# Optimization experiments

Measured on AMD Instinct MI355X. Metric: run time of the kernel, lower is better.

## Reference

```python
import jax, jax.numpy as jnp
import numpy as np

TEMP = 50.0  # softmax temperature from __init__ (temp=50.0)

N_SAMPLES = 32768
NUM_CANDIDATES = 2048
NUM_DIMS = 16


def setup_inputs() -> dict:
    key = jax.random.key(0)
    k1, k2, k3 = jax.random.split(key, 3)
    X = jax.random.normal(k1, (N_SAMPLES, NUM_DIMS), dtype=jnp.float32)
    Y = jax.random.normal(k2, (1, NUM_CANDIDATES, NUM_DIMS), dtype=jnp.float32)  # Y_rest param
    b = jax.random.normal(k3, (1, NUM_CANDIDATES), dtype=jnp.float32) * 0.1     # intercept_rest param
    return {"X": X, "Y": Y, "b": b}


def reference(X, Y, b):
    """FiniteModel.forward in convex mode with soft selection.

    scores[n, c] = <X[n], Y[0, c]> - b[0, c]           (dot-product kernel)
    weights      = softmax(temp * scores, axis=1)       (moded_max, soft mode)
    f_x[n]       = sum_c weights[n, c] * scores[n, c]
    choice[n, :] = sum_c weights[n, c] * Y[0, c, :]
    Returns (choice, f_x) as in the torch forward.
    """
    Yc = Y[0]                                     # [C, D]
    scores = jnp.einsum('nd,cd->nc', X, Yc) - b   # [N, C] (b broadcasts from [1, C])
    weights = jax.nn.softmax(TEMP * scores, axis=1)
    f_x = jnp.sum(weights * scores, axis=1)       # [N]
    choice = jnp.einsum('nc,cd->nd', weights, Yc) # [N, D]
    return choice, f_x
```

## Files before the change

kernel.cpp:

```cpp
#include <hip/hip_runtime.h>
#include <math.h>

#if defined(__has_builtin)
#  if __has_builtin(__builtin_amdgcn_exp2f)
#    define EXP2F(x) __builtin_amdgcn_exp2f(x)
#  else
#    define EXP2F(x) exp2f(x)
#  endif
#else
#  define EXP2F(x) exp2f(x)
#endif

constexpr int   DD = 16;
constexpr float T2 = 72.13475204444817f;
constexpr float DEFER_THR = 8.0f;

typedef __attribute__((ext_vector_type(8)))  short s16x8;
typedef __attribute__((ext_vector_type(16))) float f32x16;

static __device__ __forceinline__ s16x8 mk8(unsigned a, unsigned b, unsigned c, unsigned d) {
    union { unsigned u[4]; s16x8 v; } x;
    x.u[0] = a; x.u[1] = b; x.u[2] = c; x.u[3] = d;
    return x.v;
}
static __device__ __forceinline__ unsigned pack_tr(float a, float b) {
    return (__float_as_uint(a) >> 16) | (__float_as_uint(b) & 0xFFFF0000u);
}
static __device__ __forceinline__ float trunc_bf(float a) {
    return __uint_as_float(__float_as_uint(a) & 0xFFFF0000u);
}
static __device__ __forceinline__ unsigned short rne16(float f) {
    unsigned u = __float_as_uint(f);
    return (unsigned short)((u + 0x7FFFu + ((u >> 16) & 1u)) >> 16);
}
static __device__ __forceinline__ float bfh2f(unsigned short h) {
    return __uint_as_float(((unsigned)h) << 16);
}

__global__ void prep_kernel(const float* __restrict__ Y, const float* __restrict__ B,
                            unsigned short* __restrict__ YhA, unsigned short* __restrict__ YlA,
                            unsigned short* __restrict__ VhP, unsigned short* __restrict__ VlP,
                            unsigned* __restrict__ Bq, int C)
{
    int c = blockIdx.x * blockDim.x + threadIdx.x;
    if (c >= C) return;

    int c15 = c & 15;
    int j    = (c15 & 3) | (((c15 >> 3) & 1) << 2);
    int hslt = (c15 >> 2) & 1;
    int slot = (c & ~15) | (hslt << 3) | j;

    const float* yr = Y + (size_t)c * DD;
#pragma unroll
    for (int d = 0; d < DD; ++d) {
        float y = yr[d];
        unsigned short h = rne16(y);
        unsigned short l = rne16(y - bfh2f(h));
        YhA[(size_t)c * DD + d] = h;
        YlA[(size_t)c * DD + d] = l;
        VhP[(size_t)d * C + slot] = h;
        VlP[(size_t)d * C + slot] = l;
    }
    float bb = B[c];
    unsigned short bh = rne16(bb);
    VhP[(size_t)16 * C + slot] = bh;
    VlP[(size_t)16 * C + slot] = rne16(bb - bfh2f(bh));
    VhP[(size_t)17 * C + slot] = 0x3F80;
    VlP[(size_t)17 * C + slot] = 0;
#pragma unroll
    for (int r = 18; r < 32; ++r) {
        VhP[(size_t)r * C + slot] = 0;
        VlP[(size_t)r * C + slot] = 0;
    }

    float qb = -T2 * bb;
    unsigned short qh = rne16(qb);
    unsigned short ql = rne16(qb - bfh2f(qh));
    Bq[c] = (unsigned)qh | ((unsigned)ql << 16);
}

struct Frag {
    s16x8 aYh, aYl, vh0, vh1, vl0, vl1;
    unsigned bw;
};

__global__ __launch_bounds__(256, 4)
void finite_mfma(const float* __restrict__ X,
                 const unsigned short* __restrict__ YhA, const unsigned short* __restrict__ YlA,
                 const unsigned short* __restrict__ VhP, const unsigned short* __restrict__ VlP,
                 const unsigned* __restrict__ Bq,
                 float* __restrict__ out, int N, int C)
{
    const int tid  = threadIdx.x;
    const int wave = tid >> 6, lane = tid & 63;
    const int s = lane & 31, hi = lane >> 5;
    const int n0 = blockIdx.x * 32;
    const int cpw = C >> 2, cbase = wave * cpw, ntile = cpw >> 5;

    __shared__ float bufc[4][18][32];
    __shared__ float lds_m[4][32];

    const unsigned short* pYh = YhA + ((size_t)(cbase + s) * DD + 8 * hi);
    const unsigned short* pYl = YlA + ((size_t)(cbase + s) * DD + 8 * hi);
    const unsigned short* pVh = VhP + ((size_t)s * C + cbase + 8 * hi);
    const unsigned short* pVl = VlP + ((size_t)s * C + cbase + 8 * hi);
    const unsigned*       pBq = Bq + cbase + s;

    const float* xp = X + ((size_t)(n0 + s) * DD + 8 * hi);
    float xq[8];
#pragma unroll
    for (int jj = 0; jj < 8; ++jj) xq[jj] = xp[jj] * T2;
    unsigned xhw[4], xlw[4];
#pragma unroll
    for (int jj = 0; jj < 4; ++jj) {
        float a = xq[2 * jj], b = xq[2 * jj + 1];
        xhw[jj] = pack_tr(a, b);
        xlw[jj] = pack_tr(a - trunc_bf(a), b - trunc_bf(b));
    }
    const s16x8 xqh = mk8(xhw[0], xhw[1], xhw[2], xhw[3]);
    const s16x8 xql = mk8(xlw[0], xlw[1], xlw[2], xlw[3]);
    const s16x8 ones2 = mk8(hi ? 0u : 0x3F803F80u, 0u, 0u, 0u);

    f32x16 acc;
#pragma unroll
    for (int r = 0; r < 16; ++r) acc[r] = 0.0f;
    float m2 = -INFINITY;

#define LDF(F, k) do {                                              \
        (F).aYh = *(const s16x8*)(pYh + (size_t)(k) * 512);         \
        (F).aYl = *(const s16x8*)(pYl + (size_t)(k) * 512);         \
        (F).vh0 = *(const s16x8*)(pVh + (size_t)(k) * 32);          \
        (F).vh1 = *(const s16x8*)(pVh + (size_t)(k) * 32 + 16);     \
        (F).vl0 = *(const s16x8*)(pVl + (size_t)(k) * 32);          \
        (F).vl1 = *(const s16x8*)(pVl + (size_t)(k) * 32 + 16);     \
        (F).bw  = pBq[(size_t)(k) * 32];                            \
    } while (0)

#define PROC(F) do {                                                            \
        const s16x8 a2 = mk8(hi ? 0u : (F).bw, 0u, 0u, 0u);                     \
        f32x16 S;                                                               \
        _Pragma("unroll")                                                       \
        for (int r = 0; r < 16; ++r) S[r] = 0.0f;                               \
        S = __builtin_amdgcn_mfma_f32_32x32x16_bf16(a2,     ones2, S, 0, 0, 0); \
        S = __builtin_amdgcn_mfma_f32_32x32x16_bf16((F).aYh, xqh,  S, 0, 0, 0); \
        S = __builtin_amdgcn_mfma_f32_32x32x16_bf16((F).aYh, xql,  S, 0, 0, 0); \
        S = __builtin_amdgcn_mfma_f32_32x32x16_bf16((F).aYl, xqh,  S, 0, 0, 0); \
        float tmax = S[0];                                                      \
        _Pragma("unroll")                                                       \
        for (int r = 1; r < 16; ++r) tmax = fmaxf(tmax, S[r]);                  \
        tmax = fmaxf(tmax, __shfl_xor(tmax, 32, 64));                           \
        if (__any(tmax > m2 + DEFER_THR)) {                                     \
            float nm = fmaxf(m2, tmax);                                         \
            float sc = EXP2F(m2 - nm);                                          \
            _Pragma("unroll")                                                   \
            for (int r = 0; r < 16; ++r) acc[r] *= sc;                          \
            m2 = nm;                                                            \
        }                                                                       \
        unsigned phw[8], plw[8];                                                \
        _Pragma("unroll")                                                       \
        for (int jj = 0; jj < 8; ++jj) {                                        \
            float e0 = EXP2F(S[2 * jj] - m2);                                   \
            float e1 = EXP2F(S[2 * jj + 1] - m2);                               \
            phw[jj] = pack_tr(e0, e1);                                          \
            plw[jj] = pack_tr(e0 - trunc_bf(e0), e1 - trunc_bf(e1));            \
        }                                                                       \
        const s16x8 Bph0 = mk8(phw[0], phw[1], phw[2], phw[3]);                 \
        const s16x8 Bpl0 = mk8(plw[0], plw[1], plw[2], plw[3]);                 \
        const s16x8 Bph1 = mk8(phw[4], phw[5], phw[6], phw[7]);                 \
        const s16x8 Bpl1 = mk8(plw[4], plw[5], plw[6], plw[7]);                 \
        acc = __builtin_amdgcn_mfma_f32_32x32x16_bf16((F).vh0, Bph0, acc, 0, 0, 0); \
        acc = __builtin_amdgcn_mfma_f32_32x32x16_bf16((F).vl0, Bph0, acc, 0, 0, 0); \
        acc = __builtin_amdgcn_mfma_f32_32x32x16_bf16((F).vh0, Bpl0, acc, 0, 0, 0); \
        acc = __builtin_amdgcn_mfma_f32_32x32x16_bf16((F).vh1, Bph1, acc, 0, 0, 0); \
        acc = __builtin_amdgcn_mfma_f32_32x32x16_bf16((F).vl1, Bph1, acc, 0, 0, 0); \
        acc = __builtin_amdgcn_mfma_f32_32x32x16_bf16((F).vh1, Bpl1, acc, 0, 0, 0); \
    } while (0)

    Frag f0, f1;
    LDF(f0, 0);
    for (int t = 0; t < ntile; t += 2) {
        LDF(f1, t + 1);
        PROC(f0);
        if (t + 2 < ntile) LDF(f0, t + 2);
        PROC(f1);
    }
#undef LDF
#undef PROC

    if (hi == 0) lds_m[wave][s] = m2;
    __syncthreads();
    float mstar = fmaxf(fmaxf(lds_m[0][s], lds_m[1][s]), fmaxf(lds_m[2][s], lds_m[3][s]));
    float sw = EXP2F(m2 - mstar);
#pragma unroll
    for (int r = 0; r < 8; ++r) {
        int dv = (r & 3) + 8 * (r >> 2) + 4 * hi;
        bufc[wave][dv][s] = acc[r] * sw;
    }
    if (hi == 0) {
        bufc[wave][16][s] = acc[8] * sw;
        bufc[wave][17][s] = acc[9] * sw;
    }
    __syncthreads();

#pragma unroll
    for (int q = 0; q < 3; ++q) {
        int u = tid + 256 * q;
        if (u < 18 * 32) {
            int dv = u >> 5, ss = u & 31;
            bufc[0][dv][ss] = bufc[0][dv][ss] + bufc[1][dv][ss]
                            + bufc[2][dv][ss] + bufc[3][dv][ss];
        }
    }
    __syncthreads();

    {
        int ss = tid >> 3, d0 = (tid & 7) * 2;
        float inv = 1.0f / bufc[0][17][ss];
        float2 o = make_float2(bufc[0][d0][ss] * inv, bufc[0][d0 + 1][ss] * inv);
        *(float2*)(out + (size_t)(n0 + ss) * DD + d0) = o;
    }
    if (tid < 32) {
        float inv = 1.0f / bufc[0][17][tid];
        const float* xr = X + (size_t)(n0 + tid) * DD;
        float dot = 0.0f;
#pragma unroll
        for (int d = 0; d < DD; ++d) dot = fmaf(xr[d], bufc[0][d][tid], dot);
        out[(size_t)N * DD + n0 + tid] = (dot - bufc[0][16][tid]) * inv;
    }
}

extern "C" void kernel_launch(void* const* d_in, const int* in_sizes, int n_in,
                              void* d_out, int out_size, void* d_ws, size_t ws_size,
                              hipStream_t stream) {
    const float* X = (const float*)d_in[0];
    const float* Y = (const float*)d_in[1];
    const float* B = (const float*)d_in[2];
    float*     out = (float*)d_out;

    const int N = in_sizes[0] / DD;
    const int C = in_sizes[2];

    char* w = (char*)d_ws;
    unsigned short* YhA = (unsigned short*)(w);
    unsigned short* YlA = (unsigned short*)(w + (size_t)C * DD * 2);
    unsigned short* VhP = (unsigned short*)(w + (size_t)C * DD * 4);
    unsigned short* VlP = (unsigned short*)(w + (size_t)C * DD * 4 + (size_t)32 * C * 2);
    unsigned*       Bq  = (unsigned*)   (w + (size_t)C * DD * 4 + (size_t)32 * C * 4);

    hipLaunchKernelGGL(prep_kernel, dim3((C + 255) / 256), dim3(256), 0, stream,
                       Y, B, YhA, YlA, VhP, VlP, Bq, C);
    hipLaunchKernelGGL(finite_mfma, dim3(N / 32), dim3(256), 0, stream,
                       X, YhA, YlA, VhP, VlP, Bq, out, N, C);
}
```

Measured before the change: 95.73 us.

## Drop low-part softmax weight MFMAs and retile V into per-tile contiguous layout

Removes the bf16 low-part split of the exponentiated weights, cutting the second-stage MFMAs per tile from six to four and dropping the residual packing ALU work. The V operand is re-laid out so each 32-candidate tile is a contiguous 32x32 block, written with vector stores in prep and read with contiguous loads in the main kernel. The per-tile max reduction becomes a tree instead of a linear chain. Accuracy of the weighted sums drops, since the weights now carry only bf16 precision.

Result: faster. 86.74 us (-9.4%).

```diff
diff --git a/kernel.cpp b/kernel.cpp
--- a/kernel.cpp
+++ b/kernel.cpp
@@ -39,44 +39,51 @@
 
 __global__ void prep_kernel(const float* __restrict__ Y, const float* __restrict__ B,
                             unsigned short* __restrict__ YhA, unsigned short* __restrict__ YlA,
-                            unsigned short* __restrict__ VhP, unsigned short* __restrict__ VlP,
+                            unsigned short* __restrict__ V3h, unsigned short* __restrict__ V3l,
                             unsigned* __restrict__ Bq, int C)
 {
     int c = blockIdx.x * blockDim.x + threadIdx.x;
     if (c >= C) return;
 
-    int c15 = c & 15;
-    int j    = (c15 & 3) | (((c15 >> 3) & 1) << 2);
-    int hslt = (c15 >> 2) & 1;
-    int slot = (c & ~15) | (hslt << 3) | j;
-
+    union { unsigned short u[DD]; s16x8 v[2]; } hb, lb;
     const float* yr = Y + (size_t)c * DD;
 #pragma unroll
     for (int d = 0; d < DD; ++d) {
         float y = yr[d];
         unsigned short h = rne16(y);
-        unsigned short l = rne16(y - bfh2f(h));
-        YhA[(size_t)c * DD + d] = h;
-        YlA[(size_t)c * DD + d] = l;
-        VhP[(size_t)d * C + slot] = h;
-        VlP[(size_t)d * C + slot] = l;
-    }
+        hb.u[d] = h;
+        lb.u[d] = rne16(y - bfh2f(h));
+    }
+    s16x8* yh = (s16x8*)(YhA + (size_t)c * DD);
+    s16x8* yl = (s16x8*)(YlA + (size_t)c * DD);
+    yh[0] = hb.v[0]; yh[1] = hb.v[1];
+    yl[0] = lb.v[0]; yl[1] = lb.v[1];
+
     float bb = B[c];
-    unsigned short bh = rne16(bb);
-    VhP[(size_t)16 * C + slot] = bh;
-    VlP[(size_t)16 * C + slot] = rne16(bb - bfh2f(bh));
-    VhP[(size_t)17 * C + slot] = 0x3F80;
-    VlP[(size_t)17 * C + slot] = 0;
-#pragma unroll
-    for (int r = 18; r < 32; ++r) {
-        VhP[(size_t)r * C + slot] = 0;
-        VlP[(size_t)r * C + slot] = 0;
-    }
-
     float qb = -T2 * bb;
     unsigned short qh = rne16(qb);
-    unsigned short ql = rne16(qb - bfh2f(qh));
-    Bq[c] = (unsigned)qh | ((unsigned)ql << 16);
+    Bq[c] = (unsigned)qh | ((unsigned)rne16(qb - bfh2f(qh)) << 16);
+
+    const int t = c >> 5, r = c & 31;
+    union { unsigned short u[32]; s16x8 v[4]; } vh, vl;
+#pragma unroll
+    for (int slot = 0; slot < 32; ++slot) {
+        int j = slot & 7, hs = (slot >> 3) & 1;
+        int cl = (slot & 16) | (j & 3) | (hs << 2) | (((j >> 2) & 1) << 3);
+        int cc = (t << 5) | cl;
+        float v;
+        if (r < DD)            v = Y[(size_t)cc * DD + r];
+        else if (r == DD)      v = B[cc];
+        else if (r == DD + 1)  v = 1.0f;
+        else                   v = 0.0f;
+        unsigned short h = rne16(v);
+        vh.u[slot] = h;
+        vl.u[slot] = rne16(v - bfh2f(h));
+    }
+    s16x8* ph = (s16x8*)(V3h + ((size_t)t * 32 + r) * 32);
+    s16x8* pl = (s16x8*)(V3l + ((size_t)t * 32 + r) * 32);
+#pragma unroll
+    for (int q = 0; q < 4; ++q) { ph[q] = vh.v[q]; pl[q] = vl.v[q]; }
 }
 
 struct Frag {
@@ -87,7 +94,7 @@
 __global__ __launch_bounds__(256, 4)
 void finite_mfma(const float* __restrict__ X,
                  const unsigned short* __restrict__ YhA, const unsigned short* __restrict__ YlA,
-                 const unsigned short* __restrict__ VhP, const unsigned short* __restrict__ VlP,
+                 const unsigned short* __restrict__ V3h, const unsigned short* __restrict__ V3l,
                  const unsigned* __restrict__ Bq,
                  float* __restrict__ out, int N, int C)
 {
@@ -102,8 +109,8 @@
 
     const unsigned short* pYh = YhA + ((size_t)(cbase + s) * DD + 8 * hi);
     const unsigned short* pYl = YlA + ((size_t)(cbase + s) * DD + 8 * hi);
-    const unsigned short* pVh = VhP + ((size_t)s * C + cbase + 8 * hi);
-    const unsigned short* pVl = VlP + ((size_t)s * C + cbase + 8 * hi);
+    const unsigned short* pVh = V3h + (((size_t)(cbase >> 5) * 32 + s) * 32 + 8 * hi);
+    const unsigned short* pVl = V3l + (((size_t)(cbase >> 5) * 32 + s) * 32 + 8 * hi);
     const unsigned*       pBq = Bq + cbase + s;
 
     const float* xp = X + ((size_t)(n0 + s) * DD + 8 * hi);
@@ -129,10 +136,10 @@
 #define LDF(F, k) do {                                              \
         (F).aYh = *(const s16x8*)(pYh + (size_t)(k) * 512);         \
         (F).aYl = *(const s16x8*)(pYl + (size_t)(k) * 512);         \
-        (F).vh0 = *(const s16x8*)(pVh + (size_t)(k) * 32);          \
-        (F).vh1 = *(const s16x8*)(pVh + (size_t)(k) * 32 + 16);     \
-        (F).vl0 = *(const s16x8*)(pVl + (size_t)(k) * 32);          \
-        (F).vl1 = *(const s16x8*)(pVl + (size_t)(k) * 32 + 16);     \
+        (F).vh0 = *(const s16x8*)(pVh + (size_t)(k) * 1024);        \
+        (F).vh1 = *(const s16x8*)(pVh + (size_t)(k) * 1024 + 16);   \
+        (F).vl0 = *(const s16x8*)(pVl + (size_t)(k) * 1024);        \
+        (F).vl1 = *(const s16x8*)(pVl + (size_t)(k) * 1024 + 16);   \
         (F).bw  = pBq[(size_t)(k) * 32];                            \
     } while (0)
 
@@ -145,10 +152,13 @@
         S = __builtin_amdgcn_mfma_f32_32x32x16_bf16((F).aYh, xqh,  S, 0, 0, 0); \
         S = __builtin_amdgcn_mfma_f32_32x32x16_bf16((F).aYh, xql,  S, 0, 0, 0); \
         S = __builtin_amdgcn_mfma_f32_32x32x16_bf16((F).aYl, xqh,  S, 0, 0, 0); \
-        float tmax = S[0];                                                      \
-        _Pragma("unroll")                                                       \
-        for (int r = 1; r < 16; ++r) tmax = fmaxf(tmax, S[r]);                  \
-        tmax = fmaxf(tmax, __shfl_xor(tmax, 32, 64));                           \
+        float tm[8];                                                            \
+        _Pragma("unroll")                                                       \
+        for (int jj = 0; jj < 8; ++jj) tm[jj] = fmaxf(S[2 * jj], S[2 * jj + 1]);\
+        _Pragma("unroll")                                                       \
+        for (int jj = 0; jj < 4; ++jj) tm[jj] = fmaxf(tm[jj], tm[jj + 4]);      \
+        tm[0] = fmaxf(fmaxf(tm[0], tm[2]), fmaxf(tm[1], tm[3]));                \
+        float tmax = fmaxf(tm[0], __shfl_xor(tm[0], 32, 64));                   \
         if (__any(tmax > m2 + DEFER_THR)) {                                     \
             float nm = fmaxf(m2, tmax);                                         \
             float sc = EXP2F(m2 - nm);                                          \
@@ -156,24 +166,19 @@
             for (int r = 0; r < 16; ++r) acc[r] *= sc;                          \
             m2 = nm;                                                            \
         }                                                                       \
-        unsigned phw[8], plw[8];                                                \
+        unsigned phw[8];                                                        \
         _Pragma("unroll")                                                       \
         for (int jj = 0; jj < 8; ++jj) {                                        \
             float e0 = EXP2F(S[2 * jj] - m2);                                   \
             float e1 = EXP2F(S[2 * jj + 1] - m2);                               \
             phw[jj] = pack_tr(e0, e1);                                          \
-            plw[jj] = pack_tr(e0 - trunc_bf(e0), e1 - trunc_bf(e1));            \
         }                                                                       \
         const s16x8 Bph0 = mk8(phw[0], phw[1], phw[2], phw[3]);                 \
-        const s16x8 Bpl0 = mk8(plw[0], plw[1], plw[2], plw[3]);                 \
         const s16x8 Bph1 = mk8(phw[4], phw[5], phw[6], phw[7]);                 \
-        const s16x8 Bpl1 = mk8(plw[4], plw[5], plw[6], plw[7]);                 \
         acc = __builtin_amdgcn_mfma_f32_32x32x16_bf16((F).vh0, Bph0, acc, 0, 0, 0); \
         acc = __builtin_amdgcn_mfma_f32_32x32x16_bf16((F).vl0, Bph0, acc, 0, 0, 0); \
-        acc = __builtin_amdgcn_mfma_f32_32x32x16_bf16((F).vh0, Bpl0, acc, 0, 0, 0); \
         acc = __builtin_amdgcn_mfma_f32_32x32x16_bf16((F).vh1, Bph1, acc, 0, 0, 0); \
         acc = __builtin_amdgcn_mfma_f32_32x32x16_bf16((F).vl1, Bph1, acc, 0, 0, 0); \
-        acc = __builtin_amdgcn_mfma_f32_32x32x16_bf16((F).vh1, Bpl1, acc, 0, 0, 0); \
     } while (0)
 
     Frag f0, f1;
@@ -243,12 +248,12 @@
     char* w = (char*)d_ws;
     unsigned short* YhA = (unsigned short*)(w);
     unsigned short* YlA = (unsigned short*)(w + (size_t)C * DD * 2);
-    unsigned short* VhP = (unsigned short*)(w + (size_t)C * DD * 4);
-    unsigned short* VlP = (unsigned short*)(w + (size_t)C * DD * 4 + (size_t)32 * C * 2);
+    unsigned short* V3h = (unsigned short*)(w + (size_t)C * DD * 4);
+    unsigned short* V3l = (unsigned short*)(w + (size_t)C * DD * 4 + (size_t)32 * C * 2);
     unsigned*       Bq  = (unsigned*)   (w + (size_t)C * DD * 4 + (size_t)32 * C * 4);
 
     hipLaunchKernelGGL(prep_kernel, dim3((C + 255) / 256), dim3(256), 0, stream,
-                       Y, B, YhA, YlA, VhP, VlP, Bq, C);
+                       Y, B, YhA, YlA, V3h, V3l, Bq, C);
     hipLaunchKernelGGL(finite_mfma, dim3(N / 32), dim3(256), 0, stream,
-                       X, YhA, YlA, VhP, VlP, Bq, out, N, C);
-}
+                       X, YhA, YlA, V3h, V3l, Bq, out, N, C);
+}
```
